# Optimization experiments

Measured on AMD Instinct MI355X. Metric: run time of the kernel, lower is better.

## Reference

```python
import jax, jax.numpy as jnp
import numpy as np

B, H, W = 16, 544, 960
DISP_MAX = 64.0


def setup_inputs() -> dict:
    key = jax.random.key(0)
    k1, k2, k3, k4 = jax.random.split(key, 4)
    dl = jax.random.uniform(k1, (B, 1, H, W), dtype=jnp.float32) * DISP_MAX
    seg_r = jax.random.normal(k2, (B, 1, H, W), dtype=jnp.float32)
    dlgt = jax.random.uniform(k3, (B, H, W), dtype=jnp.float32) * DISP_MAX
    lgt = jax.random.normal(k4, (B, 1, H, W), dtype=jnp.float32)
    return {"dl": dl, "seg_r": seg_r, "dlgt": dlgt, "lgt": lgt}


def _warp(x, disp):
    """Disparity warp: sample x at (h, w - disp) with horizontal bilinear
    interpolation and zeros padding (grid_sample equivalent; y is untouched
    so the vertical weights collapse to 1)."""
    Bc, C, Hc, Wc = x.shape
    cols = jnp.arange(Wc, dtype=x.dtype)  # [W]
    sx = cols[None, None, None, :] - disp  # [B,1,H,W] sampling x-coord
    x0 = jnp.floor(sx)
    wx = sx - x0  # fractional part, carries grad wrt disp
    x0i = x0.astype(jnp.int32)
    x1i = x0i + 1
    v0m = ((x0i >= 0) & (x0i < Wc)).astype(x.dtype)
    v1m = ((x1i >= 0) & (x1i < Wc)).astype(x.dtype)
    x0c = jnp.clip(x0i, 0, Wc - 1)
    x1c = jnp.clip(x1i, 0, Wc - 1)
    # gather along width; C == 1 broadcasts against disp's channel dim
    g0 = jnp.take_along_axis(x, jnp.broadcast_to(x0c, x.shape), axis=-1)
    g1 = jnp.take_along_axis(x, jnp.broadcast_to(x1c, x.shape), axis=-1)
    return (1.0 - wx) * g0 * v0m + wx * g1 * v1m


def _smooth_l1(d):
    ad = jnp.abs(d)
    return jnp.where(ad < 1.0, 0.5 * d * d, ad - 0.5)


def reference(dl, seg_r, dlgt, lgt):
    mask = lgt > 0  # [B,1,H,W] bool
    mf = mask.astype(dl.dtype)
    cnt = mf.sum()
    recon_l = jax.nn.sigmoid(_warp(seg_r, dl))
    # masked-mean smooth L1 == mean over boolean-selected elements
    loss_recon = (_smooth_l1(recon_l - lgt) * mf).sum() / cnt
    loss = (_smooth_l1(dl - dlgt[:, None, :, :]) * mf).sum() / cnt
    loss = jnp.where(jnp.isnan(loss), jnp.zeros_like(loss), loss)
    return loss + 0.5 * loss_recon
```

## Files before the change

kernel.cpp:

```cpp
#include <hip/hip_runtime.h>
#include <math.h>

#define W 960
#define W4 240
#define NROWS (16 * 544)
#define ROWS_PB 4
#define NBLOCKS (NROWS / ROWS_PB)
#define LDS_STRIDE 964

__device__ __forceinline__ float smooth_l1f(float d) {
    float ad = fabsf(d);
    return ad < 1.0f ? 0.5f * d * d : ad - 0.5f;
}

__global__ __launch_bounds__(256) void loss_kernel(
    const float* __restrict__ dl,
    const float* __restrict__ seg_r,
    const float* __restrict__ dlgt,
    const float* __restrict__ lgt,
    double* __restrict__ ws)
{
    __shared__ float srow[ROWS_PB * LDS_STRIDE];
    const int tid   = threadIdx.x;
    const int base4 = blockIdx.x * (ROWS_PB * W4);

    for (int t = tid; t < ROWS_PB * W4; t += 256) {
        float4 v = ((const float4*)seg_r)[base4 + t];
        int r = t / W4;
        int c = t - r * W4;
        float* dst = &srow[r * LDS_STRIDE + (c << 2)];
        dst[0] = v.x; dst[1] = v.y; dst[2] = v.z; dst[3] = v.w;
    }
    __syncthreads();

    float cnt = 0.f, s_loss = 0.f, s_recon = 0.f;
    for (int t = tid; t < ROWS_PB * W4; t += 256) {
        int r  = t / W4;
        int c4 = t - r * W4;
        int g4 = base4 + t;
        float4 d4 = ((const float4*)dl)[g4];
        float4 l4 = ((const float4*)lgt)[g4];
        float4 t4 = ((const float4*)dlgt)[g4];
        const float* __restrict__ lrow = &srow[r * LDS_STRIDE];

        float dv[4] = {d4.x, d4.y, d4.z, d4.w};
        float lv[4] = {l4.x, l4.y, l4.z, l4.w};
        float tv[4] = {t4.x, t4.y, t4.z, t4.w};

        #pragma unroll
        for (int k = 0; k < 4; ++k) {
            float m = lv[k] > 0.f ? 1.f : 0.f;
            cnt += m;
            float d = dv[k];
            s_loss += m * smooth_l1f(d - tv[k]);

            float sx  = (float)((c4 << 2) + k) - d;
            float x0f = floorf(sx);
            float wx  = sx - x0f;
            int x0 = (int)x0f;
            int x1 = x0 + 1;
            float m0 = (x0 >= 0 && x0 < W) ? 1.f : 0.f;
            float m1 = (x1 >= 0 && x1 < W) ? 1.f : 0.f;
            int x0c = min(max(x0, 0), W - 1);
            int x1c = min(max(x1, 0), W - 1);
            float g0 = lrow[x0c] * m0;
            float g1 = lrow[x1c] * m1;
            float wv = (1.f - wx) * g0 + wx * g1;
            float recon = 1.f / (1.f + __expf(-wv));
            s_recon += m * smooth_l1f(recon - lv[k]);
        }
    }

    double dc = (double)cnt, dlo = (double)s_loss, dre = (double)s_recon;
    for (int off = 32; off > 0; off >>= 1) {
        dc  += __shfl_down(dc,  off, 64);
        dlo += __shfl_down(dlo, off, 64);
        dre += __shfl_down(dre, off, 64);
    }
    __shared__ double sh[3][4];
    int lane = tid & 63, wid = tid >> 6;
    if (lane == 0) { sh[0][wid] = dc; sh[1][wid] = dlo; sh[2][wid] = dre; }
    __syncthreads();
    if (tid == 0) {
        double c = 0, l = 0, r = 0;
        #pragma unroll
        for (int j = 0; j < 4; ++j) { c += sh[0][j]; l += sh[1][j]; r += sh[2][j]; }
        ws[blockIdx.x]               = c;
        ws[NBLOCKS + blockIdx.x]     = l;
        ws[2 * NBLOCKS + blockIdx.x] = r;
    }
}

__global__ __launch_bounds__(256) void finalize_kernel(
    const double* __restrict__ ws, float* __restrict__ out)
{
    double c = 0, l = 0, r = 0;
    for (int i = threadIdx.x; i < NBLOCKS; i += 256) {
        c += ws[i];
        l += ws[NBLOCKS + i];
        r += ws[2 * NBLOCKS + i];
    }
    for (int off = 32; off > 0; off >>= 1) {
        c += __shfl_down(c, off, 64);
        l += __shfl_down(l, off, 64);
        r += __shfl_down(r, off, 64);
    }
    __shared__ double sh[3][4];
    int lane = threadIdx.x & 63, wid = threadIdx.x >> 6;
    if (lane == 0) { sh[0][wid] = c; sh[1][wid] = l; sh[2][wid] = r; }
    __syncthreads();
    if (threadIdx.x == 0) {
        double cc = 0, ll = 0, rr = 0;
        #pragma unroll
        for (int j = 0; j < 4; ++j) { cc += sh[0][j]; ll += sh[1][j]; rr += sh[2][j]; }
        double loss = ll / cc;
        if (isnan(loss)) loss = 0.0;
        out[0] = (float)(loss + 0.5 * (rr / cc));
    }
}

extern "C" void kernel_launch(void* const* d_in, const int* in_sizes, int n_in,
                              void* d_out, int out_size, void* d_ws, size_t ws_size,
                              hipStream_t stream) {
    const float* dl    = (const float*)d_in[0];
    const float* seg_r = (const float*)d_in[1];
    const float* dlgt  = (const float*)d_in[2];
    const float* lgt   = (const float*)d_in[3];
    double* ws = (double*)d_ws;

    loss_kernel<<<NBLOCKS, 256, 0, stream>>>(dl, seg_r, dlgt, lgt, ws);
    finalize_kernel<<<1, 256, 0, stream>>>(ws, (float*)d_out);
}
```

Baseline: 156.9 us.

## Prefetch all tile loads before LDS staging and fuse finalize via atomics

All global loads for the block (seg_r plus dl, lgt, dlgt) are now issued into registers up front, before the LDS write and barrier, so memory latency overlaps instead of being serialized around the sync. The separate finalize kernel is removed. Each block now atomically adds its partial sums into three doubles, and the last block, found with an arrival counter, computes the final loss. A memset of the workspace is added per launch. This adds register pressure, 2176 blocks contending on the same atomics, and a run-to-run nondeterministic summation order.

New measurement: 259.8 us. 1.66x slower.

```diff
diff --git a/kernel.cpp b/kernel.cpp
--- a/kernel.cpp
+++ b/kernel.cpp
@@ -7,6 +7,7 @@
 #define ROWS_PB 4
 #define NBLOCKS (NROWS / ROWS_PB)
 #define LDS_STRIDE 964
+#define PBV4 (ROWS_PB * W4)
 
 __device__ __forceinline__ float smooth_l1f(float d) {
     float ad = fabsf(d);
@@ -18,56 +19,75 @@
     const float* __restrict__ seg_r,
     const float* __restrict__ dlgt,
     const float* __restrict__ lgt,
-    double* __restrict__ ws)
+    double* __restrict__ ws,
+    float* __restrict__ out)
 {
     __shared__ float srow[ROWS_PB * LDS_STRIDE];
     const int tid   = threadIdx.x;
-    const int base4 = blockIdx.x * (ROWS_PB * W4);
+    const int base4 = blockIdx.x * PBV4;
 
-    for (int t = tid; t < ROWS_PB * W4; t += 256) {
-        float4 v = ((const float4*)seg_r)[base4 + t];
-        int r = t / W4;
-        int c = t - r * W4;
-        float* dst = &srow[r * LDS_STRIDE + (c << 2)];
-        dst[0] = v.x; dst[1] = v.y; dst[2] = v.z; dst[3] = v.w;
+    float4 stg[4], dv4[4], lv4[4], tv4[4];
+    #pragma unroll
+    for (int j = 0; j < 4; ++j) {
+        int t = tid + j * 256;
+        if (t < PBV4) stg[j] = ((const float4*)seg_r)[base4 + t];
+    }
+    #pragma unroll
+    for (int j = 0; j < 4; ++j) {
+        int t = tid + j * 256;
+        if (t < PBV4) {
+            dv4[j] = ((const float4*)dl)[base4 + t];
+            lv4[j] = ((const float4*)lgt)[base4 + t];
+            tv4[j] = ((const float4*)dlgt)[base4 + t];
+        }
+    }
+
+    #pragma unroll
+    for (int j = 0; j < 4; ++j) {
+        int t = tid + j * 256;
+        if (t < PBV4) {
+            int r = t / W4;
+            int c = t - r * W4;
+            float* dst = &srow[r * LDS_STRIDE + (c << 2)];
+            float4 v = stg[j];
+            dst[0] = v.x; dst[1] = v.y; dst[2] = v.z; dst[3] = v.w;
+        }
     }
     __syncthreads();
 
     float cnt = 0.f, s_loss = 0.f, s_recon = 0.f;
-    for (int t = tid; t < ROWS_PB * W4; t += 256) {
-        int r  = t / W4;
-        int c4 = t - r * W4;
-        int g4 = base4 + t;
-        float4 d4 = ((const float4*)dl)[g4];
-        float4 l4 = ((const float4*)lgt)[g4];
-        float4 t4 = ((const float4*)dlgt)[g4];
-        const float* __restrict__ lrow = &srow[r * LDS_STRIDE];
+    #pragma unroll
+    for (int j = 0; j < 4; ++j) {
+        int t = tid + j * 256;
+        if (t < PBV4) {
+            int r  = t / W4;
+            int c4 = t - r * W4;
+            const float* __restrict__ lrow = &srow[r * LDS_STRIDE];
+            float dv[4] = {dv4[j].x, dv4[j].y, dv4[j].z, dv4[j].w};
+            float lv[4] = {lv4[j].x, lv4[j].y, lv4[j].z, lv4[j].w};
+            float tv[4] = {tv4[j].x, tv4[j].y, tv4[j].z, tv4[j].w};
+            #pragma unroll
+            for (int k = 0; k < 4; ++k) {
+                float m = lv[k] > 0.f ? 1.f : 0.f;
+                cnt += m;
+                float d = dv[k];
+                s_loss += m * smooth_l1f(d - tv[k]);
 
-        float dv[4] = {d4.x, d4.y, d4.z, d4.w};
-        float lv[4] = {l4.x, l4.y, l4.z, l4.w};
-        float tv[4] = {t4.x, t4.y, t4.z, t4.w};
-
-        #pragma unroll
-        for (int k = 0; k < 4; ++k) {
-            float m = lv[k] > 0.f ? 1.f : 0.f;
-            cnt += m;
-            float d = dv[k];
-            s_loss += m * smooth_l1f(d - tv[k]);
-
-            float sx  = (float)((c4 << 2) + k) - d;
-            float x0f = floorf(sx);
-            float wx  = sx - x0f;
-            int x0 = (int)x0f;
-            int x1 = x0 + 1;
-            float m0 = (x0 >= 0 && x0 < W) ? 1.f : 0.f;
-            float m1 = (x1 >= 0 && x1 < W) ? 1.f : 0.f;
-            int x0c = min(max(x0, 0), W - 1);
-            int x1c = min(max(x1, 0), W - 1);
-            float g0 = lrow[x0c] * m0;
-            float g1 = lrow[x1c] * m1;
-            float wv = (1.f - wx) * g0 + wx * g1;
-            float recon = 1.f / (1.f + __expf(-wv));
-            s_recon += m * smooth_l1f(recon - lv[k]);
+                float sx  = (float)((c4 << 2) + k) - d;
+                float x0f = floorf(sx);
+                float wx  = sx - x0f;
+                int x0 = (int)x0f;
+                int x1 = x0 + 1;
+                float m0 = (x0 >= 0 && x0 < W) ? 1.f : 0.f;
+                float m1 = (x1 >= 0 && x1 < W) ? 1.f : 0.f;
+                int x0c = min(max(x0, 0), W - 1);
+                int x1c = min(max(x1, 0), W - 1);
+                float g0 = lrow[x0c] * m0;
+                float g1 = lrow[x1c] * m1;
+                float wv = (1.f - wx) * g0 + wx * g1;
+                float recon = 1.f / (1.f + __expf(-wv));
+                s_recon += m * smooth_l1f(recon - lv[k]);
+            }
         }
     }
 
@@ -81,41 +101,25 @@
     int lane = tid & 63, wid = tid >> 6;
     if (lane == 0) { sh[0][wid] = dc; sh[1][wid] = dlo; sh[2][wid] = dre; }
     __syncthreads();
+
     if (tid == 0) {
         double c = 0, l = 0, r = 0;
         #pragma unroll
         for (int j = 0; j < 4; ++j) { c += sh[0][j]; l += sh[1][j]; r += sh[2][j]; }
-        ws[blockIdx.x]               = c;
-        ws[NBLOCKS + blockIdx.x]     = l;
-        ws[2 * NBLOCKS + blockIdx.x] = r;
-    }
-}
-
-__global__ __launch_bounds__(256) void finalize_kernel(
-    const double* __restrict__ ws, float* __restrict__ out)
-{
-    double c = 0, l = 0, r = 0;
-    for (int i = threadIdx.x; i < NBLOCKS; i += 256) {
-        c += ws[i];
-        l += ws[NBLOCKS + i];
-        r += ws[2 * NBLOCKS + i];
-    }
-    for (int off = 32; off > 0; off >>= 1) {
-        c += __shfl_down(c, off, 64);
-        l += __shfl_down(l, off, 64);
-        r += __shfl_down(r, off, 64);
-    }
-    __shared__ double sh[3][4];
-    int lane = threadIdx.x & 63, wid = threadIdx.x >> 6;
-    if (lane == 0) { sh[0][wid] = c; sh[1][wid] = l; sh[2][wid] = r; }
-    __syncthreads();
-    if (threadIdx.x == 0) {
-        double cc = 0, ll = 0, rr = 0;
-        #pragma unroll
-        for (int j = 0; j < 4; ++j) { cc += sh[0][j]; ll += sh[1][j]; rr += sh[2][j]; }
-        double loss = ll / cc;
-        if (isnan(loss)) loss = 0.0;
-        out[0] = (float)(loss + 0.5 * (rr / cc));
+        atomicAdd(&ws[0], c);
+        atomicAdd(&ws[1], l);
+        atomicAdd(&ws[2], r);
+        unsigned* cntp = (unsigned*)(ws + 3);
+        unsigned prev = __hip_atomic_fetch_add(cntp, 1u, __ATOMIC_ACQ_REL,
+                                               __HIP_MEMORY_SCOPE_AGENT);
+        if (prev == NBLOCKS - 1) {
+            double cc = __hip_atomic_load(&ws[0], __ATOMIC_RELAXED, __HIP_MEMORY_SCOPE_AGENT);
+            double ll = __hip_atomic_load(&ws[1], __ATOMIC_RELAXED, __HIP_MEMORY_SCOPE_AGENT);
+            double rr = __hip_atomic_load(&ws[2], __ATOMIC_RELAXED, __HIP_MEMORY_SCOPE_AGENT);
+            double loss = ll / cc;
+            if (isnan(loss)) loss = 0.0;
+            out[0] = (float)(loss + 0.5 * (rr / cc));
+        }
     }
 }
 
@@ -128,6 +132,6 @@
     const float* lgt   = (const float*)d_in[3];
     double* ws = (double*)d_ws;
 
-    loss_kernel<<<NBLOCKS, 256, 0, stream>>>(dl, seg_r, dlgt, lgt, ws);
-    finalize_kernel<<<1, 256, 0, stream>>>(ws, (float*)d_out);
+    hipMemsetAsync(d_ws, 0, 32, stream);
+    loss_kernel<<<NBLOCKS, 256, 0, stream>>>(dl, seg_r, dlgt, lgt, ws, (float*)d_out);
 }
```
